# Optimization experiments

Measured on AMD Instinct MI355X. Metric: run time of the kernel, lower is better.

The kernel has to match this reference:

```python
import jax, jax.numpy as jnp
import numpy as np

N = 8192
D_IN = 128
D_OUT = 128
EPS = 1e-06


def setup_inputs() -> dict:
    key = jax.random.key(0)
    k1, k2, k3, k4 = jax.random.split(key, 4)
    x = jax.random.normal(k1, (N, D_IN), dtype=jnp.float32)
    adj = jax.random.uniform(k2, (N, N), dtype=jnp.float32)
    # nn.Linear(in_features, out_features) params, PyTorch default-ish init scale
    bound = 1.0 / np.sqrt(D_IN)
    W = jax.random.uniform(k3, (D_OUT, D_IN), dtype=jnp.float32, minval=-bound, maxval=bound)
    b = jax.random.uniform(k4, (D_OUT,), dtype=jnp.float32, minval=-bound, maxval=bound)
    return {"x": x, "adj": adj, "W": W, "b": b}


def reference(x, adj, W, b):
    # D^{-1/2} A D^{-1/2}: the diag-matmul chain is mathematically a
    # row/col broadcast scale of adj, so express it that way (same math).
    d_inv_sqrt = 1.0 / jnp.sqrt(adj.sum(axis=1) + EPS)  # [N]
    adj_norm = d_inv_sqrt[:, None] * adj * d_inv_sqrt[None, :]  # [N, N]
    h = adj_norm @ x  # [N, D_IN]
    return h @ W.T + b  # [N, D_OUT]
```

## Files before the change

### kernel.cpp

```cpp
#include <hip/hip_runtime.h>
#include <hip/hip_bf16.h>

#define NN 8192
#define DIN 128
#define DOUT 128

typedef __bf16 bf16;
typedef __bf16 bf16x8 __attribute__((ext_vector_type(8)));
typedef float f32x4 __attribute__((ext_vector_type(4)));

__global__ __launch_bounds__(256) void k1_rowsum(const float* __restrict__ adj,
                                                 float* __restrict__ dinv) {
    int row = blockIdx.x;
    int t   = threadIdx.x;
    const float4* p = reinterpret_cast<const float4*>(adj + (size_t)row * NN);
    float s = 0.f;
    #pragma unroll
    for (int i = 0; i < 8; ++i) {
        float4 v = p[t + i * 256];
        s += (v.x + v.y) + (v.z + v.w);
    }
    #pragma unroll
    for (int off = 32; off > 0; off >>= 1) s += __shfl_down(s, off, 64);
    __shared__ float r4[4];
    if ((t & 63) == 0) r4[t >> 6] = s;
    __syncthreads();
    if (t == 0) dinv[row] = rsqrtf(((r4[0] + r4[1]) + (r4[2] + r4[3])) + 1e-6f);
}

__global__ __launch_bounds__(256) void k2_xwT(const float* __restrict__ x,
                                              const float* __restrict__ W,
                                              const float* __restrict__ dinv,
                                              bf16* __restrict__ yT) {
    __shared__ float Wl[128 * 132];
    __shared__ float xl[32 * 132];
    __shared__ float dl[32];
    int t  = threadIdx.x;
    int i0 = blockIdx.x * 32;
    if (t < 32) dl[t] = dinv[i0 + t];
    #pragma unroll
    for (int s = 0; s < 16; ++s) {
        int i  = t + s * 256;
        int o  = i >> 5;
        int c4 = i & 31;
        *reinterpret_cast<float4*>(&Wl[o * 132 + c4 * 4]) =
            *reinterpret_cast<const float4*>(W + o * 128 + c4 * 4);
    }
    #pragma unroll
    for (int s = 0; s < 4; ++s) {
        int i   = t + s * 256;
        int row = i >> 5;
        int c4  = i & 31;
        *reinterpret_cast<float4*>(&xl[row * 132 + c4 * 4]) =
            *reinterpret_cast<const float4*>(x + (size_t)(i0 + row) * DIN + c4 * 4);
    }
    __syncthreads();
    int o = t & 127;
    int g = t >> 7;
    float acc[16] = {};
    for (int c4 = 0; c4 < 32; ++c4) {
        float4 w4 = *reinterpret_cast<const float4*>(&Wl[o * 132 + c4 * 4]);
        #pragma unroll
        for (int r = 0; r < 16; ++r) {
            float4 h4 = *reinterpret_cast<const float4*>(&xl[(g * 16 + r) * 132 + c4 * 4]);
            acc[r] += h4.x * w4.x + h4.y * w4.y + h4.z * w4.z + h4.w * w4.w;
        }
    }
    bf16x8 o0, o1;
    #pragma unroll
    for (int r = 0; r < 8; ++r) o0[r] = (bf16)(acc[r] * dl[g * 16 + r]);
    #pragma unroll
    for (int r = 0; r < 8; ++r) o1[r] = (bf16)(acc[8 + r] * dl[g * 16 + 8 + r]);
    bf16* dst = yT + (size_t)o * NN + i0 + g * 16;
    *reinterpret_cast<bf16x8*>(dst)     = o0;
    *reinterpret_cast<bf16x8*>(dst + 8) = o1;
}

__global__ __launch_bounds__(256) void k0_init(const float* __restrict__ bias,
                                               float* __restrict__ out) {
    int g = blockIdx.x * 256 + threadIdx.x;
    float4 b4 = *reinterpret_cast<const float4*>(bias + (threadIdx.x & 31) * 4);
    *reinterpret_cast<float4*>(out + (size_t)g * 4) = b4;
}

#define KR 512
#define LDB3 520

__global__ __launch_bounds__(512, 2) void k3_spmm(const float* __restrict__ adj,
                                                  const bf16* __restrict__ yT,
                                                  const float* __restrict__ dinv,
                                                  float* __restrict__ out) {
    __shared__ bf16 BL[128 * LDB3];
    int t     = threadIdx.x;
    int split = blockIdx.x & 15;
    int mg    = blockIdx.x >> 4;
    int m0    = mg * 256;
    int k0    = split * KR;
    for (int i = t; i < 128 * 64; i += 512) {
        int c = i >> 6, ch = i & 63;
        *reinterpret_cast<uint4*>(&BL[c * LDB3 + ch * 8]) =
            *reinterpret_cast<const uint4*>(yT + (size_t)c * NN + k0 + ch * 8);
    }
    __syncthreads();

    int wave = t >> 6, lane = t & 63;
    int mrow = lane & 15, quad = lane >> 4;
    int wm0  = wave * 32 + m0;

    f32x4 dv0 = *reinterpret_cast<const f32x4*>(dinv + wm0 + quad * 4);
    f32x4 dv1 = *reinterpret_cast<const f32x4*>(dinv + wm0 + 16 + quad * 4);

    f32x4 acc[2][8] = {};
    const float* a0p = adj + (size_t)(wm0 + mrow) * NN + k0 + quad * 8;
    const float* a1p = a0p + (size_t)16 * NN;

    float4 c0a = *(const float4*)a0p;       float4 c0b = *(const float4*)(a0p + 4);
    float4 c1a = *(const float4*)a1p;       float4 c1b = *(const float4*)(a1p + 4);

    for (int kk = 0; kk < KR / 32; ++kk) {
        bf16x8 bf[8];
        int boff = kk * 32 + quad * 8;
        #pragma unroll
        for (int nt = 0; nt < 8; ++nt)
            bf[nt] = *reinterpret_cast<const bf16x8*>(&BL[(nt * 16 + mrow) * LDB3 + boff]);
        float4 n0a, n0b, n1a, n1b;
        if (kk < KR / 32 - 1) {
            const float* p0 = a0p + (kk + 1) * 32;
            const float* p1 = a1p + (kk + 1) * 32;
            n0a = *(const float4*)p0; n0b = *(const float4*)(p0 + 4);
            n1a = *(const float4*)p1; n1b = *(const float4*)(p1 + 4);
        }
        bf16x8 af0 = { (bf16)c0a.x, (bf16)c0a.y, (bf16)c0a.z, (bf16)c0a.w,
                       (bf16)c0b.x, (bf16)c0b.y, (bf16)c0b.z, (bf16)c0b.w };
        bf16x8 af1 = { (bf16)c1a.x, (bf16)c1a.y, (bf16)c1a.z, (bf16)c1a.w,
                       (bf16)c1b.x, (bf16)c1b.y, (bf16)c1b.z, (bf16)c1b.w };
        #pragma unroll
        for (int nt = 0; nt < 8; ++nt) {
            acc[0][nt] = __builtin_amdgcn_mfma_f32_16x16x32_bf16(af0, bf[nt], acc[0][nt], 0, 0, 0);
            acc[1][nt] = __builtin_amdgcn_mfma_f32_16x16x32_bf16(af1, bf[nt], acc[1][nt], 0, 0, 0);
        }
        c0a = n0a; c0b = n0b; c1a = n1a; c1b = n1b;
    }
    #pragma unroll
    for (int nt = 0; nt < 8; ++nt) {
        int col = nt * 16 + mrow;
        #pragma unroll
        for (int r = 0; r < 4; ++r) {
            unsafeAtomicAdd(out + (size_t)(wm0 + quad * 4 + r) * DOUT + col,
                            acc[0][nt][r] * dv0[r]);
            unsafeAtomicAdd(out + (size_t)(wm0 + 16 + quad * 4 + r) * DOUT + col,
                            acc[1][nt][r] * dv1[r]);
        }
    }
}

extern "C" void kernel_launch(void* const* d_in, const int* in_sizes, int n_in,
                              void* d_out, int out_size, void* d_ws, size_t ws_size,
                              hipStream_t stream) {
    const float* x   = (const float*)d_in[0];
    const float* adj = (const float*)d_in[1];
    const float* W   = (const float*)d_in[2];
    const float* b   = (const float*)d_in[3];
    float* out = (float*)d_out;
    char* ws = (char*)d_ws;
    float* dinv = (float*)ws;
    bf16*  yT   = (bf16*)(ws + (1u << 20));

    k1_rowsum<<<NN, 256, 0, stream>>>(adj, dinv);
    k2_xwT   <<<NN / 32, 256, 0, stream>>>(x, W, dinv, yT);
    k0_init  <<<(NN * DOUT / 4) / 256, 256, 0, stream>>>(b, out);
    k3_spmm  <<<16 * (NN / 256), 512, 0, stream>>>(adj, yT, dinv, out);
}
```

Baseline: 463.9 us.

## Replace atomic split-K accumulation with partial buffers and a separate reduce kernel

The SpMM kernel now uses 4 K-splits of 2048 instead of 16 of 512. Each block covers 128 rows, one 16-row tile per wave, and loops over four 512-wide chunks of yT staged in LDS, prefetching adj two steps ahead. Partial results are written with plain stores to a workspace buffer, and a new reduce kernel sums the four partials and adds the bias. This removes the bias-init kernel and the float atomics into the output. In exchange it adds extra workspace traffic, more LDS reloads of yT per block, and half the MFMA work per wave per A-fragment load.

```diff
diff --git a/kernel.cpp b/kernel.cpp
--- a/kernel.cpp
+++ b/kernel.cpp
@@ -76,82 +76,82 @@
     *reinterpret_cast<bf16x8*>(dst + 8) = o1;
 }
 
-__global__ __launch_bounds__(256) void k0_init(const float* __restrict__ bias,
-                                               float* __restrict__ out) {
-    int g = blockIdx.x * 256 + threadIdx.x;
-    float4 b4 = *reinterpret_cast<const float4*>(bias + (threadIdx.x & 31) * 4);
-    *reinterpret_cast<float4*>(out + (size_t)g * 4) = b4;
-}
-
-#define KR 512
+#define KR3 512
 #define LDB3 520
 
 __global__ __launch_bounds__(512, 2) void k3_spmm(const float* __restrict__ adj,
                                                   const bf16* __restrict__ yT,
                                                   const float* __restrict__ dinv,
-                                                  float* __restrict__ out) {
+                                                  float* __restrict__ part) {
     __shared__ bf16 BL[128 * LDB3];
     int t     = threadIdx.x;
-    int split = blockIdx.x & 15;
-    int mg    = blockIdx.x >> 4;
-    int m0    = mg * 256;
-    int k0    = split * KR;
-    for (int i = t; i < 128 * 64; i += 512) {
-        int c = i >> 6, ch = i & 63;
-        *reinterpret_cast<uint4*>(&BL[c * LDB3 + ch * 8]) =
-            *reinterpret_cast<const uint4*>(yT + (size_t)c * NN + k0 + ch * 8);
-    }
-    __syncthreads();
+    int split = blockIdx.x & 3;
+    int mg    = blockIdx.x >> 2;
+    int m0    = mg * 128;
+    int kbase = split * 2048;
 
     int wave = t >> 6, lane = t & 63;
     int mrow = lane & 15, quad = lane >> 4;
-    int wm0  = wave * 32 + m0;
+    int wm0  = m0 + wave * 16;
 
-    f32x4 dv0 = *reinterpret_cast<const f32x4*>(dinv + wm0 + quad * 4);
-    f32x4 dv1 = *reinterpret_cast<const f32x4*>(dinv + wm0 + 16 + quad * 4);
+    f32x4 acc[8] = {};
 
-    f32x4 acc[2][8] = {};
-    const float* a0p = adj + (size_t)(wm0 + mrow) * NN + k0 + quad * 8;
-    const float* a1p = a0p + (size_t)16 * NN;
+    for (int cc = 0; cc < 4; ++cc) {
+        int kc = kbase + cc * KR3;
+        if (cc) __syncthreads();
+        for (int i = t; i < 128 * 64; i += 512) {
+            int c = i >> 6, ch = i & 63;
+            *reinterpret_cast<uint4*>(&BL[c * LDB3 + ch * 8]) =
+                *reinterpret_cast<const uint4*>(yT + (size_t)c * NN + kc + ch * 8);
+        }
+        __syncthreads();
 
-    float4 c0a = *(const float4*)a0p;       float4 c0b = *(const float4*)(a0p + 4);
-    float4 c1a = *(const float4*)a1p;       float4 c1b = *(const float4*)(a1p + 4);
+        const float* ap = adj + (size_t)(wm0 + mrow) * NN + kc + quad * 8;
+        float4 c0 = *(const float4*)(ap);
+        float4 c1 = *(const float4*)(ap + 4);
+        float4 n0 = *(const float4*)(ap + 32);
+        float4 n1 = *(const float4*)(ap + 36);
+        #pragma unroll
+        for (int kk = 0; kk < KR3 / 32; ++kk) {
+            bf16x8 bf[8];
+            int boff = kk * 32 + quad * 8;
+            #pragma unroll
+            for (int nt = 0; nt < 8; ++nt)
+                bf[nt] = *reinterpret_cast<const bf16x8*>(&BL[(nt * 16 + mrow) * LDB3 + boff]);
+            int pk = (kk < KR3 / 32 - 2) ? (kk + 2) * 32 : 0;
+            float4 f0 = *(const float4*)(ap + pk);
+            float4 f1 = *(const float4*)(ap + pk + 4);
+            bf16x8 af = { (bf16)c0.x, (bf16)c0.y, (bf16)c0.z, (bf16)c0.w,
+                          (bf16)c1.x, (bf16)c1.y, (bf16)c1.z, (bf16)c1.w };
+            #pragma unroll
+            for (int nt = 0; nt < 8; ++nt)
+                acc[nt] = __builtin_amdgcn_mfma_f32_16x16x32_bf16(af, bf[nt], acc[nt], 0, 0, 0);
+            c0 = n0; c1 = n1; n0 = f0; n1 = f1;
+        }
+    }
 
-    for (int kk = 0; kk < KR / 32; ++kk) {
-        bf16x8 bf[8];
-        int boff = kk * 32 + quad * 8;
-        #pragma unroll
-        for (int nt = 0; nt < 8; ++nt)
-            bf[nt] = *reinterpret_cast<const bf16x8*>(&BL[(nt * 16 + mrow) * LDB3 + boff]);
-        float4 n0a, n0b, n1a, n1b;
-        if (kk < KR / 32 - 1) {
-            const float* p0 = a0p + (kk + 1) * 32;
-            const float* p1 = a1p + (kk + 1) * 32;
-            n0a = *(const float4*)p0; n0b = *(const float4*)(p0 + 4);
-            n1a = *(const float4*)p1; n1b = *(const float4*)(p1 + 4);
-        }
-        bf16x8 af0 = { (bf16)c0a.x, (bf16)c0a.y, (bf16)c0a.z, (bf16)c0a.w,
-                       (bf16)c0b.x, (bf16)c0b.y, (bf16)c0b.z, (bf16)c0b.w };
-        bf16x8 af1 = { (bf16)c1a.x, (bf16)c1a.y, (bf16)c1a.z, (bf16)c1a.w,
-                       (bf16)c1b.x, (bf16)c1b.y, (bf16)c1b.z, (bf16)c1b.w };
-        #pragma unroll
-        for (int nt = 0; nt < 8; ++nt) {
-            acc[0][nt] = __builtin_amdgcn_mfma_f32_16x16x32_bf16(af0, bf[nt], acc[0][nt], 0, 0, 0);
-            acc[1][nt] = __builtin_amdgcn_mfma_f32_16x16x32_bf16(af1, bf[nt], acc[1][nt], 0, 0, 0);
-        }
-        c0a = n0a; c0b = n0b; c1a = n1a; c1b = n1b;
-    }
+    f32x4 dv = *reinterpret_cast<const f32x4*>(dinv + wm0 + quad * 4);
+    float* pout = part + (size_t)split * (NN * DOUT) + (size_t)wm0 * DOUT;
     #pragma unroll
     for (int nt = 0; nt < 8; ++nt) {
         int col = nt * 16 + mrow;
         #pragma unroll
-        for (int r = 0; r < 4; ++r) {
-            unsafeAtomicAdd(out + (size_t)(wm0 + quad * 4 + r) * DOUT + col,
-                            acc[0][nt][r] * dv0[r]);
-            unsafeAtomicAdd(out + (size_t)(wm0 + 16 + quad * 4 + r) * DOUT + col,
-                            acc[1][nt][r] * dv1[r]);
-        }
+        for (int r = 0; r < 4; ++r)
+            pout[(quad * 4 + r) * DOUT + col] = acc[nt][r] * dv[r];
     }
+}
+
+__global__ __launch_bounds__(256) void k4_reduce(const float* __restrict__ part,
+                                                 const float* __restrict__ bias,
+                                                 float* __restrict__ out) {
+    size_t g = (size_t)blockIdx.x * 256 + threadIdx.x;
+    float4 s = *reinterpret_cast<const float4*>(bias + (g & 31) * 4);
+    #pragma unroll
+    for (int sp = 0; sp < 4; ++sp) {
+        float4 p = *reinterpret_cast<const float4*>(part + (size_t)sp * NN * DOUT + g * 4);
+        s.x += p.x; s.y += p.y; s.z += p.z; s.w += p.w;
+    }
+    *reinterpret_cast<float4*>(out + g * 4) = s;
 }
 
 extern "C" void kernel_launch(void* const* d_in, const int* in_sizes, int n_in,
@@ -165,9 +165,10 @@
     char* ws = (char*)d_ws;
     float* dinv = (float*)ws;
     bf16*  yT   = (bf16*)(ws + (1u << 20));
+    float* part = (float*)(ws + (4u << 20));
 
     k1_rowsum<<<NN, 256, 0, stream>>>(adj, dinv);
     k2_xwT   <<<NN / 32, 256, 0, stream>>>(x, W, dinv, yT);
-    k0_init  <<<(NN * DOUT / 4) / 256, 256, 0, stream>>>(b, out);
-    k3_spmm  <<<16 * (NN / 256), 512, 0, stream>>>(adj, yT, dinv, out);
+    k3_spmm  <<<4 * (NN / 128), 512, 0, stream>>>(adj, yT, dinv, part);
+    k4_reduce<<<(NN * DOUT / 4) / 256, 256, 0, stream>>>(part, b, out);
 }
```

After: 445.6 us. 3.9% less time.
